# Kernel tuning notes

Measured on AMD Instinct MI355X. Metric: run time of the kernel, lower is better.

## Reference

```python
import jax, jax.numpy as jnp
import numpy as np

B, S, E, H = 4, 1024, 1024, 16
HD = E // H
MAX_SEQ = 5000


def setup_inputs() -> dict:
    key = jax.random.key(0)
    ks = jax.random.split(key, 10)
    def lin(kw, kb):
        w = jax.random.normal(kw, (E, E), dtype=jnp.float32) * (1.0 / np.sqrt(E))
        b = jax.random.normal(kb, (E,), dtype=jnp.float32) * 0.01
        return w, b
    wq, bq = lin(ks[0], ks[1])
    wk, bk = lin(ks[2], ks[3])
    wv, bv = lin(ks[4], ks[5])
    wo, bo = lin(ks[6], ks[7])
    rpe_table = jax.random.normal(ks[8], (H, 2 * MAX_SEQ - 1, HD), dtype=jnp.float32) * 0.02
    x = jax.random.normal(ks[9], (B, S, E), dtype=jnp.float32)
    return {"x": x, "wq": wq, "bq": bq, "wk": wk, "bk": bk,
            "wv": wv, "bv": bv, "wo": wo, "bo": bo, "rpe_table": rpe_table}


def reference(x, wq, bq, wk, bk, wv, bv, wo, bo, rpe_table):
    b, s, e = x.shape
    scale = 1.0 / np.sqrt(HD)
    # projections (torch Linear: y = x @ W^T + b), reshape to (b, h, s, hd)
    q = (x @ wq.T + bq).reshape(b, s, H, HD).transpose(0, 2, 1, 3)
    k = (x @ wk.T + bk).reshape(b, s, H, HD).transpose(0, 2, 1, 3)
    v = (x @ wv.T + bv).reshape(b, s, H, HD).transpose(0, 2, 1, 3)
    scores = jnp.einsum('bhqd,bhkd->bhqk', q, k) * scale
    # RPE: rpe[h, q, k, d] = table[h, q - k + s - 1, d]; factor the einsum:
    # rel[b,h,q,r] = sum_d q[b,h,q,d] * table[h,r,d], then gather r = q - k + s - 1
    table = rpe_table[:, : 2 * s - 1]               # (H, 2s-1, HD)
    rel = jnp.einsum('bhqd,hrd->bhqr', q, table)    # (b, H, s, 2s-1)
    idx = jnp.arange(s)[:, None] - jnp.arange(s)[None, :] + (s - 1)  # (s, s)
    rpe_scores = jnp.take_along_axis(
        rel, jnp.broadcast_to(idx[None, None], (b, H, s, s)), axis=-1)
    attn = jax.nn.softmax(scores + rpe_scores, axis=-1)
    ctx = jnp.einsum('bhqk,bhkd->bhqd', attn, v)
    ctx = ctx.transpose(0, 2, 1, 3).reshape(b, s, e)
    return ctx @ wo.T + bo
```

## Files before the change

### kernel.cpp

```cpp
#include <hip/hip_runtime.h>
#include <hip/hip_bf16.h>
#include <stdint.h>

typedef __attribute__((ext_vector_type(8))) short s8v;
typedef __attribute__((ext_vector_type(4))) float f32x4;
typedef __attribute__((ext_vector_type(16))) float f32x16;

union V16 { uint4 u4; unsigned int u[4]; s8v s; };

__device__ inline s8v u4_to_s8(uint4 v) { V16 c; c.u4 = v; return c.s; }
__device__ inline s8v words_to_s8(unsigned int a, unsigned int b, unsigned int c, unsigned int d) {
  V16 t; t.u[0] = a; t.u[1] = b; t.u[2] = c; t.u[3] = d; return t.s;
}
__device__ inline unsigned short f2b(float f) {
  __hip_bfloat16 h = __float2bfloat16(f);
  unsigned short u; __builtin_memcpy(&u, &h, 2); return u;
}
__device__ inline unsigned int pack2(float lo, float hi) {
  return ((unsigned int)f2b(hi) << 16) | (unsigned int)f2b(lo);
}
__device__ inline unsigned int cvtpk(float lo, float hi) {
  unsigned int r; asm("v_cvt_pk_bf16_f32 %0, %1, %2" : "=v"(r) : "v"(lo), "v"(hi)); return r;
}
__device__ inline float exp2_fast(float x) {
#if __has_builtin(__builtin_amdgcn_exp2f)
  return __builtin_amdgcn_exp2f(x);
#else
  float y; asm("v_exp_f32 %0, %1" : "=v"(y) : "v"(x)); return y;
#endif
}
__device__ inline void gld16(const void* g, void* lds) {
  __builtin_amdgcn_global_load_lds((const __attribute__((address_space(1))) void*)g,
                                   (__attribute__((address_space(3))) void*)lds, 16, 0, 0);
}

#define LOG2E 1.4426950408889634f

__global__ void cvt_fused_kernel(const float* __restrict__ x, const float* __restrict__ wq,
                                 const float* __restrict__ wk, const float* __restrict__ wv,
                                 const float* __restrict__ wo, const float* __restrict__ tb,
                                 __hip_bfloat16* __restrict__ XB, __hip_bfloat16* __restrict__ WQKV,
                                 __hip_bfloat16* __restrict__ WOb, __hip_bfloat16* __restrict__ TBL) {
  const int bid = blockIdx.x;
  if (bid < 4096) {
    size_t i = ((size_t)bid * 256 + threadIdx.x) * 8;
    const float* src; __hip_bfloat16* dst; size_t off;
    if (i < 4194304)      { src = x;  dst = XB;             off = i; }
    else if (i < 5242880) { src = wq; dst = WQKV;           off = i - 4194304; }
    else if (i < 6291456) { src = wk; dst = WQKV + 1048576; off = i - 5242880; }
    else if (i < 7340032) { src = wv; dst = WQKV + 2097152; off = i - 6291456; }
    else                  { src = wo; dst = WOb;            off = i - 7340032; }
    const float4* s4 = (const float4*)(src + off);
    float4 a = s4[0], b = s4[1];
    uint4 o;
    o.x = pack2(a.x, a.y); o.y = pack2(a.z, a.w);
    o.z = pack2(b.x, b.y); o.w = pack2(b.z, b.w);
    *(uint4*)(dst + off) = o;
  } else {
    size_t i = ((size_t)(bid - 4096) * 256 + threadIdx.x) * 8;
    int h = (int)(i >> 17);
    int rem = (int)(i & 131071);
    int r = rem >> 6, c = rem & 63;
    uint4 o;
    if (r < 2047) {
      const float4* s4 = (const float4*)(tb + ((size_t)h * 9999 + r) * 64 + c);
      float4 a = s4[0], b = s4[1];
      o.x = pack2(a.x * LOG2E, a.y * LOG2E); o.y = pack2(a.z * LOG2E, a.w * LOG2E);
      o.z = pack2(b.x * LOG2E, b.y * LOG2E); o.w = pack2(b.z * LOG2E, b.w * LOG2E);
    } else { o.x = 0u; o.y = 0u; o.z = 0u; o.w = 0u; }
    *(uint4*)(TBL + i) = o;
  }
}

__global__ __launch_bounds__(256, 3) void gemm_qkv(
    const __hip_bfloat16* __restrict__ A,
    const __hip_bfloat16* __restrict__ Bt,
    const float* __restrict__ bq, const float* __restrict__ bk, const float* __restrict__ bv,
    __hip_bfloat16* __restrict__ QB, __hip_bfloat16* __restrict__ KB,
    __hip_bfloat16* __restrict__ VTB) {
  __shared__ __align__(16) char smem[32768];
  char* As = smem;
  char* Bs = smem + 16384;
  const int tid = threadIdx.x;
  const int w = tid >> 6, l = tid & 63;
  const int wr = w >> 1, wc = w & 1;
  const int lr = l & 15, lg = l >> 4;
  const int m0 = blockIdx.y * 128, n0 = blockIdx.x * 128;

  f32x4 acc[4][4] = {};

  for (int kt = 0; kt < 16; ++kt) {
    __syncthreads();
    #pragma unroll
    for (int i = 0; i < 4; ++i) {
      const int off = i * 4096 + w * 1024;
      const int loff = off + l * 16;
      const int row = loff >> 7;
      const int cb = loff & 127;
      const int sc = cb ^ ((row & 7) << 4);
      gld16((const char*)A  + (size_t)(m0 + row) * 2048 + kt * 128 + sc, As + off);
      gld16((const char*)Bt + (size_t)(n0 + row) * 2048 + kt * 128 + sc, Bs + off);
    }
    asm volatile("s_waitcnt vmcnt(0)" ::: "memory");
    __syncthreads();
    #pragma unroll
    for (int ks = 0; ks < 2; ++ks) {
      uint4 af[4], bf4[4];
      #pragma unroll
      for (int i = 0; i < 4; ++i) {
        const int ra = wr * 64 + i * 16 + lr;
        const int rb = wc * 64 + i * 16 + lr;
        const int cb = ks * 64 + lg * 16;
        af[i]  = *(const uint4*)(As + ra * 128 + (cb ^ ((ra & 7) << 4)));
        bf4[i] = *(const uint4*)(Bs + rb * 128 + (cb ^ ((rb & 7) << 4)));
      }
      #pragma unroll
      for (int i = 0; i < 4; ++i) {
        #pragma unroll
        for (int j = 0; j < 4; ++j)
          acc[i][j] = __builtin_amdgcn_mfma_f32_16x16x32_bf16(u4_to_s8(af[i]), u4_to_s8(bf4[j]), acc[i][j], 0, 0, 0);
      }
    }
  }

  const int mrow = m0 + wr * 64 + lg * 4;
  const int ncol = n0 + wc * 64 + lr;
  const int cls = blockIdx.x >> 3;

  if (cls < 2) {
    const float sc = cls ? 0.125f * LOG2E : 1.0f;
    const float* bias = cls ? bk : bq;
    __hip_bfloat16* op = cls ? KB : QB;
    #pragma unroll
    for (int j = 0; j < 4; ++j) {
      const int n = ncol - cls * 1024 + j * 16;
      const float bia = bias[n];
      const int hh = n >> 6, hd = n & 63;
      #pragma unroll
      for (int i = 0; i < 4; ++i) {
        #pragma unroll
        for (int r = 0; r < 4; ++r) {
          const int m = mrow + i * 16 + r;
          const int bb = m >> 10, ss = m & 1023;
          op[(((size_t)(bb * 16 + hh)) * 1024 + ss) * 64 + hd] = __float2bfloat16((acc[i][j][r] + bia) * sc);
        }
      }
    }
  } else {
    #pragma unroll
    for (int j = 0; j < 4; ++j) {
      const int f = ncol - 2048 + j * 16;
      const float bia = bv[f];
      const int fh = f >> 6, fd = f & 63;
      #pragma unroll
      for (int i = 0; i < 4; ++i) {
        const int m = mrow + i * 16;
        const int bb = m >> 10, ss = m & 1023;
        ushort4 qv;
        qv.x = f2b(acc[i][j][0] + bia); qv.y = f2b(acc[i][j][1] + bia);
        qv.z = f2b(acc[i][j][2] + bia); qv.w = f2b(acc[i][j][3] + bia);
        *(ushort4*)((char*)VTB + (((size_t)bb * 1048576 + (size_t)fh * 65536 + fd * 1024 + ss) * 2)) = qv;
      }
    }
  }
}

__global__ __launch_bounds__(256, 3) void gemm_out(
    const __hip_bfloat16* __restrict__ A,
    const __hip_bfloat16* __restrict__ Bt,
    const float* __restrict__ bo,
    float* __restrict__ out) {
  __shared__ __align__(16) char smem[32768];
  char* As = smem;
  char* Bs = smem + 16384;
  const int tid = threadIdx.x;
  const int w = tid >> 6, l = tid & 63;
  const int wr = w >> 1, wc = w & 1;
  const int lr = l & 15, lg = l >> 4;
  const int m0 = blockIdx.y * 128, n0 = blockIdx.x * 128;

  f32x4 acc[4][4] = {};

  for (int kt = 0; kt < 16; ++kt) {
    __syncthreads();
    #pragma unroll
    for (int i = 0; i < 4; ++i) {
      const int off = i * 4096 + w * 1024;
      const int loff = off + l * 16;
      const int row = loff >> 7;
      const int cb = loff & 127;
      const int sc = cb ^ ((row & 7) << 4);
      gld16((const char*)A  + (size_t)(m0 + row) * 2048 + kt * 128 + sc, As + off);
      gld16((const char*)Bt + (size_t)(n0 + row) * 2048 + kt * 128 + sc, Bs + off);
    }
    asm volatile("s_waitcnt vmcnt(0)" ::: "memory");
    __syncthreads();
    #pragma unroll
    for (int ks = 0; ks < 2; ++ks) {
      uint4 af[4], bf4[4];
      #pragma unroll
      for (int i = 0; i < 4; ++i) {
        const int ra = wr * 64 + i * 16 + lr;
        const int rb = wc * 64 + i * 16 + lr;
        const int cb = ks * 64 + lg * 16;
        af[i]  = *(const uint4*)(As + ra * 128 + (cb ^ ((ra & 7) << 4)));
        bf4[i] = *(const uint4*)(Bs + rb * 128 + (cb ^ ((rb & 7) << 4)));
      }
      #pragma unroll
      for (int i = 0; i < 4; ++i) {
        #pragma unroll
        for (int j = 0; j < 4; ++j)
          acc[i][j] = __builtin_amdgcn_mfma_f32_16x16x32_bf16(u4_to_s8(af[i]), u4_to_s8(bf4[j]), acc[i][j], 0, 0, 0);
      }
    }
  }

  const int mrow = m0 + wr * 64 + lg * 4;
  const int ncol = n0 + wc * 64 + lr;
  #pragma unroll
  for (int j = 0; j < 4; ++j) {
    const int n = ncol + j * 16;
    const float bia = bo[n];
    #pragma unroll
    for (int i = 0; i < 4; ++i) {
      #pragma unroll
      for (int r = 0; r < 4; ++r) {
        const int m = mrow + i * 16 + r;
        out[(size_t)m * 1024 + n] = acc[i][j][r] + bia;
      }
    }
  }
}

__global__ __launch_bounds__(256, 2) void attn_kernel(
    const __hip_bfloat16* __restrict__ Qg,
    const __hip_bfloat16* __restrict__ Kg,
    const __hip_bfloat16* __restrict__ VTg,
    const __hip_bfloat16* __restrict__ Tg,
    __hip_bfloat16* __restrict__ Cg) {
  __shared__ __align__(16) char smem[81920];
  char* Klds = smem;
  char* Tlds = smem + 16384;
  const int tid = threadIdx.x;
  const int w = tid >> 6, l = tid & 63;
  const int ql = l & 31, half = l >> 5;
  char* relw = smem + 49152 + w * 8192;

  const int bx = blockIdx.x;
  const int work = (bx & 7) * 64 + (bx >> 3);
  const int b = work & 3, hqt = work >> 2;
  const int h = hqt >> 3, qt = hqt & 7;
  const int qb = qt * 128;
  const int q0 = qb + 32 * w;

  const size_t bh = (size_t)(b * 16 + h);
  const char* Qb = (const char*)Qg + bh * 131072;
  const char* Kb = (const char*)Kg + bh * 131072;
  const char* Vb = (const char*)VTg + bh * 131072;
  const char* Tb = (const char*)Tg + (size_t)h * 262144;

  const int relsw = ql * 256 + ((ql & 15) << 4);
  const int u4 = (ql << 2) - (half << 4);
  const int k0sw = ql * 128 + ((ql & 7) << 4);
  const int k1sw = (32 + ql) * 128 + ((ql & 7) << 4);

  auto stageK = [&](int k0n, int buf) {
    #pragma unroll
    for (int i = 0; i < 2; ++i) {
      const int loff = i * 4096 + w * 1024 + l * 16;
      const int row = loff >> 7, cb = loff & 127;
      const int sc = cb ^ ((row & 7) << 4);
      gld16(Kb + (size_t)(k0n + row) * 128 + sc, Klds + buf * 8192 + i * 4096 + w * 1024);
    }
  };
  auto stageT = [&](int rsrc, int slot) {
    char* dst = Tlds + slot * 8192;
    #pragma unroll
    for (int i = 0; i < 2; ++i) {
      const int loff = i * 4096 + w * 1024 + l * 16;
      const int row = loff >> 7, cb = loff & 127;
      const int sc = cb ^ ((row & 7) << 4);
      gld16(Tb + (size_t)(rsrc + row) * 128 + sc, dst + i * 4096 + w * 1024);
    }
  };

  s8v qv[4];
  {
    const char* qrow = Qb + (size_t)(q0 + ql) * 128 + half * 16;
    #pragma unroll
    for (int ds = 0; ds < 4; ++ds) qv[ds] = u4_to_s8(*(const uint4*)(qrow + ds * 32));
  }

  f32x16 cacc0 = {}, cacc1 = {};
  float mL = -1.0e30f, lsum = 0.0f;
  int rbase = qb + 960;

  stageK(0, 0);
  stageT(rbase,       ((rbase >> 6) + 0) & 3);
  stageT(rbase + 64,  ((rbase >> 6) + 1) & 3);
  stageT(rbase + 128, ((rbase >> 6) + 2) & 3);
  __builtin_amdgcn_sched_barrier(0);
  uint4 vr[8];
  #pragma unroll
  for (int t = 0; t < 2; ++t)
    #pragma unroll
    for (int ks = 0; ks < 4; ++ks)
      vr[t * 4 + ks] = *(const uint4*)(Vb + (size_t)(t * 32 + ql) * 2048 + ks * 32 + half * 16);
  asm volatile("s_waitcnt vmcnt(8)" ::: "memory");
  __builtin_amdgcn_s_barrier();

  for (int kt = 0; kt < 16; ++kt, rbase -= 64) {
    stageK(((kt + 1) & 15) * 64, (kt + 1) & 1);
    { const int rbn = rbase - 64;
      stageT(rbn < 0 ? 0 : rbn, (rbn >> 6) & 3); }

    const int kb = (kt & 1) * 8192;
    f32x16 p0 = {}, p1 = {};
    __builtin_amdgcn_s_setprio(1);
    #pragma unroll
    for (int ds = 0; ds < 4; ++ds) {
      const int cb = ds * 32 + half * 16;
      uint4 kf0 = *(const uint4*)(Klds + kb + (k0sw ^ cb));
      uint4 kf1 = *(const uint4*)(Klds + kb + (k1sw ^ cb));
      p0 = __builtin_amdgcn_mfma_f32_32x32x16_bf16(u4_to_s8(kf0), qv[ds], p0, 0, 0, 0);
      p1 = __builtin_amdgcn_mfma_f32_32x32x16_bf16(u4_to_s8(kf1), qv[ds], p1, 0, 0, 0);
    }
    __builtin_amdgcn_s_setprio(0);

    #pragma unroll
    for (int ti = 0; ti < 3; ++ti) {
      const int bt = (ti == 0) ? 2 : ((ti == 1) ? 0 : 1);
      const int slot = ((rbase >> 6) + ((w + bt) >> 1)) & 3;
      const int rowin = ((w + bt) & 1) * 32 + ql;
      const int tbsw = slot * 8192 + rowin * 128 + ((ql & 7) << 4);
      f32x16 racc = {};
      __builtin_amdgcn_s_setprio(1);
      #pragma unroll
      for (int ds = 0; ds < 4; ++ds) {
        const int cb = ds * 32 + half * 16;
        uint4 tf = *(const uint4*)(Tlds + (tbsw ^ cb));
        racc = __builtin_amdgcn_mfma_f32_32x32x16_bf16(u4_to_s8(tf), qv[ds], racc, 0, 0, 0);
      }
      __builtin_amdgcn_s_setprio(0);
      #pragma unroll
      for (int g = 0; g < 4; ++g) {
        #pragma unroll
        for (int j = 0; j < 4; ++j) {
          int pos4;
          if (bt == 2)      pos4 = (u4 + 4 * (-1 - j - 8 * g)) & 124;
          else if (bt == 0) pos4 = ((u4 + 4 * (63 - j - 8 * g)) & 252) | 128;
          else              pos4 = (u4 + 4 * (31 - j - 8 * g)) & 252;
          *(float*)(relw + (relsw ^ pos4)) = racc[4 * g + j];
        }
      }
    }

    #pragma unroll
    for (int mp = 0; mp < 4; ++mp) {
      const int X0 = 32 * mp + 16 * half;
      f32x4 r0 = *(const f32x4*)(relw + (relsw ^ X0));
      f32x4 r1 = *(const f32x4*)(relw + (relsw ^ (X0 + 128)));
      #pragma unroll
      for (int j = 0; j < 4; ++j) {
        p0[4 * mp + j] += r0[j];
        p1[4 * mp + j] += r1[j];
      }
    }

    float mx[8];
    #pragma unroll
    for (int i = 0; i < 8; ++i)
      mx[i] = fmaxf(fmaxf(p0[2 * i], p0[2 * i + 1]), fmaxf(p1[2 * i], p1[2 * i + 1]));
    float pmax = fmaxf(fmaxf(fmaxf(mx[0], mx[1]), fmaxf(mx[2], mx[3])),
                       fmaxf(fmaxf(mx[4], mx[5]), fmaxf(mx[6], mx[7])));
    pmax = fmaxf(pmax, __shfl_xor(pmax, 32));
    if (!__all(pmax - mL <= 12.0f)) {
      const float mnew = fmaxf(mL, pmax);
      const float corr = exp2_fast(mL - mnew);
      mL = mnew;
      lsum *= corr;
      #pragma unroll
      for (int r = 0; r < 16; ++r) {
        const float cr = __shfl(corr, (r & 3) + 8 * (r >> 2) + 4 * half);
        cacc0[r] *= cr;
        cacc1[r] *= cr;
      }
    }
    #pragma unroll
    for (int r = 0; r < 16; ++r) {
      p0[r] = exp2_fast(p0[r] - mL);
      p1[r] = exp2_fast(p1[r] - mL);
    }
    float sm[8];
    #pragma unroll
    for (int i = 0; i < 8; ++i)
      sm[i] = (p0[2 * i] + p0[2 * i + 1]) + (p1[2 * i] + p1[2 * i + 1]);
    float psum = ((sm[0] + sm[1]) + (sm[2] + sm[3])) + ((sm[4] + sm[5]) + (sm[6] + sm[7]));
    psum += __shfl_xor(psum, 32);
    lsum += psum;

    unsigned int w0[8], w1[8];
    #pragma unroll
    for (int jw = 0; jw < 8; ++jw) {
      w0[jw] = cvtpk(p0[2 * jw], p0[2 * jw + 1]);
      w1[jw] = cvtpk(p1[2 * jw], p1[2 * jw + 1]);
    }
    unsigned int r0x[4], r1x[4];
    #pragma unroll
    for (int i = 0; i < 4; ++i) {
      const int jkeep = (i & 1) + 4 * (i >> 1);
      const int jsend = jkeep + 2;
      unsigned int v0 = half ? w0[jkeep] : w0[jsend];
      unsigned int v1 = half ? w1[jkeep] : w1[jsend];
      r0x[i] = (unsigned int)__shfl_xor((int)v0, 32);
      r1x[i] = (unsigned int)__shfl_xor((int)v1, 32);
    }

    asm volatile("s_waitcnt vmcnt(4)" ::: "memory");

    __builtin_amdgcn_s_setprio(1);
    #pragma unroll
    for (int ks = 0; ks < 4; ++ks) {
      const int mm = ks & 1;
      unsigned int f0_, f1_, f2_, f3_;
      if (ks < 2) {
        f0_ = half ? r0x[2 * mm]     : w0[4 * mm];
        f1_ = half ? r0x[2 * mm + 1] : w0[4 * mm + 1];
        f2_ = half ? w0[4 * mm + 2]  : r0x[2 * mm];
        f3_ = half ? w0[4 * mm + 3]  : r0x[2 * mm + 1];
      } else {
        f0_ = half ? r1x[2 * mm]     : w1[4 * mm];
        f1_ = half ? r1x[2 * mm + 1] : w1[4 * mm + 1];
        f2_ = half ? w1[4 * mm + 2]  : r1x[2 * mm];
        f3_ = half ? w1[4 * mm + 3]  : r1x[2 * mm + 1];
      }
      s8v pf = words_to_s8(f0_, f1_, f2_, f3_);
      cacc0 = __builtin_amdgcn_mfma_f32_32x32x16_bf16(pf, u4_to_s8(vr[ks]), cacc0, 0, 0, 0);
      cacc1 = __builtin_amdgcn_mfma_f32_32x32x16_bf16(pf, u4_to_s8(vr[4 + ks]), cacc1, 0, 0, 0);
    }
    __builtin_amdgcn_s_setprio(0);

    { const int kn2 = ((kt + 1) & 15) * 128;
      #pragma unroll
      for (int t = 0; t < 2; ++t)
        #pragma unroll
        for (int ks = 0; ks < 4; ++ks)
          vr[t * 4 + ks] = *(const uint4*)(Vb + (size_t)(t * 32 + ql) * 2048 + kn2 + ks * 32 + half * 16);
    }

    asm volatile("s_waitcnt vmcnt(8)" ::: "memory");
    __builtin_amdgcn_s_barrier();
  }
  asm volatile("s_waitcnt vmcnt(0)" ::: "memory");

  #pragma unroll
  for (int r = 0; r < 16; ++r) {
    const int qr = (r & 3) + 8 * (r >> 2) + 4 * half;
    const float inv = 1.0f / __shfl(lsum, qr);
    const size_t row = (size_t)b * 1024 + q0 + qr;
    const size_t basei = row * 1024 + h * 64 + ql;
    Cg[basei]      = __float2bfloat16(cacc0[r] * inv);
    Cg[basei + 32] = __float2bfloat16(cacc1[r] * inv);
  }
}

extern "C" void kernel_launch(void* const* d_in, const int* in_sizes, int n_in,
                              void* d_out, int out_size, void* d_ws, size_t ws_size,
                              hipStream_t stream) {
  (void)in_sizes; (void)n_in; (void)out_size; (void)ws_size;
  const float* x  = (const float*)d_in[0];
  const float* wq = (const float*)d_in[1];
  const float* bq = (const float*)d_in[2];
  const float* wk = (const float*)d_in[3];
  const float* bk = (const float*)d_in[4];
  const float* wv = (const float*)d_in[5];
  const float* bv = (const float*)d_in[6];
  const float* wo = (const float*)d_in[7];
  const float* bo = (const float*)d_in[8];
  const float* tb = (const float*)d_in[9];

  char* ws = (char*)d_ws;
  __hip_bfloat16* XB   = (__hip_bfloat16*)(ws);
  __hip_bfloat16* WQKV = (__hip_bfloat16*)(ws + 8388608);
  __hip_bfloat16* WOb  = (__hip_bfloat16*)(ws + 14680064);
  __hip_bfloat16* TBL  = (__hip_bfloat16*)(ws + 16777216);
  __hip_bfloat16* QB   = (__hip_bfloat16*)(ws + 20971520);
  __hip_bfloat16* KB   = (__hip_bfloat16*)(ws + 29360128);
  __hip_bfloat16* VTB  = (__hip_bfloat16*)(ws + 37748736);
  __hip_bfloat16* CTX  = (__hip_bfloat16*)(ws + 46137344);

  cvt_fused_kernel<<<5120, 256, 0, stream>>>(x, wq, wk, wv, wo, tb, XB, WQKV, WOb, TBL);
  gemm_qkv<<<dim3(24, 32), 256, 0, stream>>>(XB, WQKV, bq, bk, bv, QB, KB, VTB);
  attn_kernel<<<512, 256, 0, stream>>>(QB, KB, VTB, TBL, CTX);
  gemm_out<<<dim3(8, 32), 256, 0, stream>>>(CTX, WOb, bo, (float*)d_out);
}
```

Before: 114.7 us.

## Cache shared RPE tile in registers and drop K/T double-buffered prefetch pipeline

The attention loop now reuses the relative-position tile computed for band 0 as band 2 of the next iteration, holding it in registers. This removes one of the three RPE MFMA tiles per iteration after the first. It also drops K double buffering and the 4-slot T ring: K uses a single buffer, T uses a 3-slot ring, LDS shrinks from 80KB to 64KB, and loads are synchronous with waitcnt(0) and two barriers per iteration. V loads are no longer prefetched a tile ahead. The smaller LDS footprint and fewer MFMAs trade against losing global-load/compute overlap.

```diff
diff --git a/kernel.cpp b/kernel.cpp
--- a/kernel.cpp
+++ b/kernel.cpp
@@ -238,13 +238,13 @@
     const __hip_bfloat16* __restrict__ VTg,
     const __hip_bfloat16* __restrict__ Tg,
     __hip_bfloat16* __restrict__ Cg) {
-  __shared__ __align__(16) char smem[81920];
+  __shared__ __align__(16) char smem[65536];
   char* Klds = smem;
-  char* Tlds = smem + 16384;
+  char* Tlds = smem + 8192;
   const int tid = threadIdx.x;
   const int w = tid >> 6, l = tid & 63;
   const int ql = l & 31, half = l >> 5;
-  char* relw = smem + 49152 + w * 8192;
+  char* relw = smem + 32768 + w * 8192;
 
   const int bx = blockIdx.x;
   const int work = (bx & 7) * 64 + (bx >> 3);
@@ -264,16 +264,17 @@
   const int k0sw = ql * 128 + ((ql & 7) << 4);
   const int k1sw = (32 + ql) * 128 + ((ql & 7) << 4);
 
-  auto stageK = [&](int k0n, int buf) {
+  auto stageK = [&](int k0n) {
     #pragma unroll
     for (int i = 0; i < 2; ++i) {
       const int loff = i * 4096 + w * 1024 + l * 16;
       const int row = loff >> 7, cb = loff & 127;
       const int sc = cb ^ ((row & 7) << 4);
-      gld16(Kb + (size_t)(k0n + row) * 128 + sc, Klds + buf * 8192 + i * 4096 + w * 1024);
+      gld16(Kb + (size_t)(k0n + row) * 128 + sc, Klds + i * 4096 + w * 1024);
     }
   };
-  auto stageT = [&](int rsrc, int slot) {
+  auto stageT = [&](int rsrc) {
+    const int slot = (int)(((unsigned)(rsrc >> 6)) % 3u);
     char* dst = Tlds + slot * 8192;
     #pragma unroll
     for (int i = 0; i < 2; ++i) {
@@ -292,45 +293,29 @@
   }
 
   f32x16 cacc0 = {}, cacc1 = {};
+  f32x16 rcache = {};
   float mL = -1.0e30f, lsum = 0.0f;
   int rbase = qb + 960;
 
-  stageK(0, 0);
-  stageT(rbase,       ((rbase >> 6) + 0) & 3);
-  stageT(rbase + 64,  ((rbase >> 6) + 1) & 3);
-  stageT(rbase + 128, ((rbase >> 6) + 2) & 3);
-  __builtin_amdgcn_sched_barrier(0);
-  uint4 vr[8];
-  #pragma unroll
-  for (int t = 0; t < 2; ++t)
-    #pragma unroll
-    for (int ks = 0; ks < 4; ++ks)
-      vr[t * 4 + ks] = *(const uint4*)(Vb + (size_t)(t * 32 + ql) * 2048 + ks * 32 + half * 16);
-  asm volatile("s_waitcnt vmcnt(8)" ::: "memory");
-  __builtin_amdgcn_s_barrier();
-
   for (int kt = 0; kt < 16; ++kt, rbase -= 64) {
-    stageK(((kt + 1) & 15) * 64, (kt + 1) & 1);
-    { const int rbn = rbase - 64;
-      stageT(rbn < 0 ? 0 : rbn, (rbn >> 6) & 3); }
-
-    const int kb = (kt & 1) * 8192;
-    f32x16 p0 = {}, p1 = {};
-    __builtin_amdgcn_s_setprio(1);
-    #pragma unroll
-    for (int ds = 0; ds < 4; ++ds) {
-      const int cb = ds * 32 + half * 16;
-      uint4 kf0 = *(const uint4*)(Klds + kb + (k0sw ^ cb));
-      uint4 kf1 = *(const uint4*)(Klds + kb + (k1sw ^ cb));
-      p0 = __builtin_amdgcn_mfma_f32_32x32x16_bf16(u4_to_s8(kf0), qv[ds], p0, 0, 0, 0);
-      p1 = __builtin_amdgcn_mfma_f32_32x32x16_bf16(u4_to_s8(kf1), qv[ds], p1, 0, 0, 0);
-    }
-    __builtin_amdgcn_s_setprio(0);
-
-    #pragma unroll
-    for (int ti = 0; ti < 3; ++ti) {
-      const int bt = (ti == 0) ? 2 : ((ti == 1) ? 0 : 1);
-      const int slot = ((rbase >> 6) + ((w + bt) >> 1)) & 3;
+    __syncthreads();
+    stageK(kt * 64);
+    stageT(rbase);
+    if (kt == 0) { stageT(rbase + 64); stageT(rbase + 128); }
+    asm volatile("s_waitcnt vmcnt(0)" ::: "memory");
+    __syncthreads();
+
+    uint4 vr[8];
+    { const int kn = kt * 128;
+      #pragma unroll
+      for (int t = 0; t < 2; ++t)
+        #pragma unroll
+        for (int ks = 0; ks < 4; ++ks)
+          vr[t * 4 + ks] = *(const uint4*)(Vb + (size_t)(t * 32 + ql) * 2048 + kn + ks * 32 + half * 16);
+    }
+
+    auto relTile = [&](int bt) {
+      const int slot = (int)(((unsigned)(rbase >> 6) + (unsigned)((w + bt) >> 1)) % 3u);
       const int rowin = ((w + bt) & 1) * 32 + ql;
       const int tbsw = slot * 8192 + rowin * 128 + ((ql & 7) << 4);
       f32x16 racc = {};
@@ -342,18 +327,46 @@
         racc = __builtin_amdgcn_mfma_f32_32x32x16_bf16(u4_to_s8(tf), qv[ds], racc, 0, 0, 0);
       }
       __builtin_amdgcn_s_setprio(0);
-      #pragma unroll
-      for (int g = 0; g < 4; ++g) {
-        #pragma unroll
-        for (int j = 0; j < 4; ++j) {
-          int pos4;
-          if (bt == 2)      pos4 = (u4 + 4 * (-1 - j - 8 * g)) & 124;
-          else if (bt == 0) pos4 = ((u4 + 4 * (63 - j - 8 * g)) & 252) | 128;
-          else              pos4 = (u4 + 4 * (31 - j - 8 * g)) & 252;
-          *(float*)(relw + (relsw ^ pos4)) = racc[4 * g + j];
-        }
-      }
-    }
+      return racc;
+    };
+
+    f32x16 racc2 = (kt == 0) ? relTile(2) : rcache;
+    #pragma unroll
+    for (int g = 0; g < 4; ++g)
+      #pragma unroll
+      for (int j = 0; j < 4; ++j) {
+        const int pos4 = (u4 + 4 * (-1 - j - 8 * g)) & 124;
+        *(float*)(relw + (relsw ^ pos4)) = racc2[4 * g + j];
+      }
+    f32x16 racc0 = relTile(0);
+    #pragma unroll
+    for (int g = 0; g < 4; ++g)
+      #pragma unroll
+      for (int j = 0; j < 4; ++j) {
+        const int pos4 = ((u4 + 4 * (63 - j - 8 * g)) & 252) | 128;
+        *(float*)(relw + (relsw ^ pos4)) = racc0[4 * g + j];
+      }
+    rcache = racc0;
+    f32x16 racc1 = relTile(1);
+    #pragma unroll
+    for (int g = 0; g < 4; ++g)
+      #pragma unroll
+      for (int j = 0; j < 4; ++j) {
+        const int pos4 = (u4 + 4 * (31 - j - 8 * g)) & 252;
+        *(float*)(relw + (relsw ^ pos4)) = racc1[4 * g + j];
+      }
+
+    f32x16 p0 = {}, p1 = {};
+    __builtin_amdgcn_s_setprio(1);
+    #pragma unroll
+    for (int ds = 0; ds < 4; ++ds) {
+      const int cb = ds * 32 + half * 16;
+      uint4 kf0 = *(const uint4*)(Klds + (k0sw ^ cb));
+      uint4 kf1 = *(const uint4*)(Klds + (k1sw ^ cb));
+      p0 = __builtin_amdgcn_mfma_f32_32x32x16_bf16(u4_to_s8(kf0), qv[ds], p0, 0, 0, 0);
+      p1 = __builtin_amdgcn_mfma_f32_32x32x16_bf16(u4_to_s8(kf1), qv[ds], p1, 0, 0, 0);
+    }
+    __builtin_amdgcn_s_setprio(0);
 
     #pragma unroll
     for (int mp = 0; mp < 4; ++mp) {
@@ -415,8 +428,6 @@
       r0x[i] = (unsigned int)__shfl_xor((int)v0, 32);
       r1x[i] = (unsigned int)__shfl_xor((int)v1, 32);
     }
-
-    asm volatile("s_waitcnt vmcnt(4)" ::: "memory");
 
     __builtin_amdgcn_s_setprio(1);
     #pragma unroll
@@ -439,19 +450,7 @@
       cacc1 = __builtin_amdgcn_mfma_f32_32x32x16_bf16(pf, u4_to_s8(vr[4 + ks]), cacc1, 0, 0, 0);
     }
     __builtin_amdgcn_s_setprio(0);
-
-    { const int kn2 = ((kt + 1) & 15) * 128;
-      #pragma unroll
-      for (int t = 0; t < 2; ++t)
-        #pragma unroll
-        for (int ks = 0; ks < 4; ++ks)
-          vr[t * 4 + ks] = *(const uint4*)(Vb + (size_t)(t * 32 + ql) * 2048 + kn2 + ks * 32 + half * 16);
-    }
-
-    asm volatile("s_waitcnt vmcnt(8)" ::: "memory");
-    __builtin_amdgcn_s_barrier();
-  }
-  asm volatile("s_waitcnt vmcnt(0)" ::: "memory");
+  }
 
   #pragma unroll
   for (int r = 0; r < 16; ++r) {
```

Result: faster. 110.1 us (-4.1%).
